# Optimization experiments

Measured on AMD Instinct MI355X. Metric: run time of the kernel, lower is better.

The kernel has to match this reference:

```python
import jax, jax.numpy as jnp
import numpy as np

NUM_HEADS = 8
HEAD_DIM = 64      # key_dim = tts_embed_dims // num_heads
TOKEN_NUM = 10
EMBED_DIMS = 512   # tts_embed_dims (num_units)
QUERY_DIM = 256    # tts_embed_dims // 2
BATCH = 131072


def setup_inputs() -> dict:
    key = jax.random.key(0)
    k1, k2, k3, k4 = jax.random.split(key, 4)
    inputs = jax.random.normal(k1, (BATCH, QUERY_DIM), dtype=jnp.float32)
    # nn.Parameter init.normal_(mean=0, std=0.5)
    embed = 0.5 * jax.random.normal(k2, (TOKEN_NUM, HEAD_DIM), dtype=jnp.float32)
    # nn.Linear weights are [out_features, in_features]
    Wq = jax.random.normal(k3, (EMBED_DIMS, QUERY_DIM), dtype=jnp.float32) * (QUERY_DIM ** -0.5)
    Wk = jax.random.normal(k4, (EMBED_DIMS, HEAD_DIM), dtype=jnp.float32) * (HEAD_DIM ** -0.5)
    return {"inputs": inputs, "embed": embed, "Wq": Wq, "Wk": Wk}


def reference(inputs, embed, Wq, Wk):
    # Faithful to this fork: values = raw tanh(embed) keys (W_value unused),
    # and NO softmax on the attention scores.
    N = inputs.shape[0]
    h, d, T = NUM_HEADS, HEAD_DIM, TOKEN_NUM
    keys_raw = jnp.tanh(embed)                       # [T, d] (shared across batch)

    q = inputs @ Wq.T                                # [N, E]
    q = q.reshape(N, h, d)                           # split heads (T_q == 1 squeezed)

    k = keys_raw @ Wk.T                              # [T, E]
    k = k.reshape(T, h, d)                           # [T, h, d]

    scale = HEAD_DIM ** 0.5                          # self.key_dim ** 0.5
    # scores: [h, N, 1, T] -> store as [h, N, T]
    scores = jnp.einsum('nhd,thd->hnt', q, k) / scale

    # out per head: scores @ values, values = keys_raw [T, d]
    out = jnp.einsum('hnt,td->nhd', scores, keys_raw)  # [N, h, d]
    style_embed = out.reshape(N, 1, h * d)             # concat heads -> [N, 1, E]
    attn_score = scores[:, :, None, :]                 # [h, N, 1, T]
    return style_embed, attn_score
```

## Files before the change

### kernel.cpp

```cpp
#include <hip/hip_runtime.h>
#include <math.h>

#define N_QDIM 256
#define N_EDIM 512
#define N_HEADS 8
#define N_HDIM 64
#define N_TOK 10
#define NJ 80

typedef short bf16x8 __attribute__((ext_vector_type(8)));
typedef float f32x4 __attribute__((ext_vector_type(4)));

__global__ __launch_bounds__(256) void precompute_kernel(
    const float* __restrict__ embed, const float* __restrict__ Wq,
    const float* __restrict__ Wk, unsigned short* __restrict__ WfHi,
    unsigned short* __restrict__ WfLo, float* __restrict__ keysOut)
{
    __shared__ float skeys[N_TOK * N_HDIM];
    __shared__ float sK[N_TOK * N_EDIM];
    const int tid = threadIdx.x;

    for (int i = tid; i < N_TOK * N_HDIM; i += 256) {
        float v = tanhf(embed[i]);
        skeys[i] = v;
        if (blockIdx.x == 0) keysOut[i] = v;
    }
    __syncthreads();

    for (int i = tid; i < N_TOK * N_EDIM; i += 256) {
        int t = i >> 9;
        int e = i & 511;
        float s = 0.f;
        #pragma unroll
        for (int d = 0; d < N_HDIM; d++)
            s += skeys[t * N_HDIM + d] * Wk[e * N_HDIM + d];
        sK[i] = s;
    }
    __syncthreads();

    int flat = blockIdx.x * 256 + tid;
    int e    = flat & 7;
    int lane = (flat >> 3) & 63;
    int rest = flat >> 9;
    int n    = rest % 5;
    int kb   = rest / 5;
    int c    = n * 16 + (lane & 15);
    int h    = c / N_TOK;
    int t    = c - h * N_TOK;
    int qd   = kb * 32 + (lane >> 4) * 8 + e;

    float s = 0.f;
    #pragma unroll
    for (int d = 0; d < N_HDIM; d++)
        s += Wq[(h * N_HDIM + d) * N_QDIM + qd] * sK[t * N_EDIM + h * N_HDIM + d];
    s *= 0.125f;

    unsigned int u = __float_as_uint(s);
    float rem = s - __uint_as_float(u & 0xffff0000u);
    int idx = ((kb * 5 + n) * 64 + lane) * 8 + e;
    WfHi[idx] = (unsigned short)(u >> 16);
    WfLo[idx] = (unsigned short)(__float_as_uint(rem) >> 16);
}

static __device__ __forceinline__ void splitFrag(float4 v0, float4 v1,
                                                 bf16x8& hi, bf16x8& lo)
{
    float x[8] = {v0.x, v0.y, v0.z, v0.w, v1.x, v1.y, v1.z, v1.w};
    #pragma unroll
    for (int e = 0; e < 8; e++) {
        unsigned u = __float_as_uint(x[e]);
        hi[e] = (short)(u >> 16);
        float r = x[e] - __uint_as_float(u & 0xffff0000u);
        lo[e] = (short)(__float_as_uint(r) >> 16);
    }
}

#define WAVE_LDS_FENCE() asm volatile("s_waitcnt lgkmcnt(0)" ::: "memory")

__global__ __launch_bounds__(256, 5) void main_kernel(
    const float* __restrict__ inputs, const unsigned short* __restrict__ WfHi,
    const unsigned short* __restrict__ WfLo, const float* __restrict__ keys,
    float* __restrict__ outStyle, float* __restrict__ outAttn, int N)
{
    __shared__ float sS[4][16 * 84];

    const int tid = threadIdx.x;
    const int w   = tid >> 6;
    const int l   = tid & 63;
    const int l15 = l & 15;
    const int lg  = l >> 4;
    const int rowBase = blockIdx.x * 128 + w * 32;

    const float* pa0 = inputs + (size_t)(rowBase + l15) * N_QDIM + lg * 8;
    const float* pa1 = pa0 + 16 * N_QDIM;

    f32x4 acc[2][5];
    #pragma unroll
    for (int m = 0; m < 2; m++)
        #pragma unroll
        for (int n = 0; n < 5; n++)
            acc[m][n] = (f32x4){0.f, 0.f, 0.f, 0.f};

    #pragma unroll 2
    for (int kb = 0; kb < 8; kb++) {
        const float* p0 = pa0 + kb * 32;
        const float* p1 = pa1 + kb * 32;
        float4 x0 = *(const float4*)(p0);
        float4 x1 = *(const float4*)(p0 + 4);
        float4 y0 = *(const float4*)(p1);
        float4 y1 = *(const float4*)(p1 + 4);
        bf16x8 a0h, a0l, a1h, a1l;
        splitFrag(x0, x1, a0h, a0l);
        splitFrag(y0, y1, a1h, a1l);

        const unsigned short* bh = WfHi + kb * 2560 + l * 8;
        const unsigned short* bl = WfLo + kb * 2560 + l * 8;
        #pragma unroll
        for (int n = 0; n < 5; n++) {
            bf16x8 bhi = *(const bf16x8*)(bh + n * 512);
            bf16x8 blo = *(const bf16x8*)(bl + n * 512);
            acc[0][n] = __builtin_amdgcn_mfma_f32_16x16x32_bf16(a0h, bhi, acc[0][n], 0, 0, 0);
            acc[1][n] = __builtin_amdgcn_mfma_f32_16x16x32_bf16(a1h, bhi, acc[1][n], 0, 0, 0);
            acc[0][n] = __builtin_amdgcn_mfma_f32_16x16x32_bf16(a0l, bhi, acc[0][n], 0, 0, 0);
            acc[1][n] = __builtin_amdgcn_mfma_f32_16x16x32_bf16(a1l, bhi, acc[1][n], 0, 0, 0);
            acc[0][n] = __builtin_amdgcn_mfma_f32_16x16x32_bf16(a0h, blo, acc[0][n], 0, 0, 0);
            acc[1][n] = __builtin_amdgcn_mfma_f32_16x16x32_bf16(a1h, blo, acc[1][n], 0, 0, 0);
        }
    }

    float* s = sS[w];

    #pragma unroll
    for (int n = 0; n < 5; n++)
        #pragma unroll
        for (int r = 0; r < 4; r++)
            s[(lg * 4 + r) * 84 + n * 16 + l15] = acc[0][n][r];
    WAVE_LDS_FENCE();

    float4 kr[N_TOK];
    #pragma unroll
    for (int t = 0; t < N_TOK; t++)
        kr[t] = *(const float4*)(keys + t * N_HDIM + l15 * 4);

    #pragma unroll
    for (int m = 0; m < 2; m++) {
        const int rStart = rowBase + m * 16;

        #pragma unroll
        for (int h = 0; h < N_HEADS; h++) {
            float* dst = outAttn + ((size_t)h * N + rStart) * N_TOK;
            #pragma unroll
            for (int it = 0; it < 3; it++) {
                int i = it * 64 + l;
                if (i < 16 * N_TOK) {
                    int rr = i / N_TOK;
                    int t  = i - rr * N_TOK;
                    __builtin_nontemporal_store(s[rr * 84 + h * N_TOK + t], dst + i);
                }
            }
        }

        #pragma unroll
        for (int i = 0; i < 4; i++) {
            int rr = i * 4 + lg;
            const float* srow = s + rr * 84;
            float* orow = outStyle + (size_t)(rStart + rr) * N_EDIM + l15 * 4;
            #pragma unroll
            for (int h = 0; h < N_HEADS; h++) {
                f32x4 o = {0.f, 0.f, 0.f, 0.f};
                #pragma unroll
                for (int t2 = 0; t2 < N_TOK; t2 += 2) {
                    float2 sc = *(const float2*)(srow + h * N_TOK + t2);
                    o[0] += sc.x * kr[t2].x + sc.y * kr[t2 + 1].x;
                    o[1] += sc.x * kr[t2].y + sc.y * kr[t2 + 1].y;
                    o[2] += sc.x * kr[t2].z + sc.y * kr[t2 + 1].z;
                    o[3] += sc.x * kr[t2].w + sc.y * kr[t2 + 1].w;
                }
                __builtin_nontemporal_store(o, (f32x4*)(orow + h * N_HDIM));
            }
        }

        if (m == 0) {
            WAVE_LDS_FENCE();
            #pragma unroll
            for (int n = 0; n < 5; n++)
                #pragma unroll
                for (int r = 0; r < 4; r++)
                    s[(lg * 4 + r) * 84 + n * 16 + l15] = acc[1][n][r];
            WAVE_LDS_FENCE();
        }
    }
}

extern "C" void kernel_launch(void* const* d_in, const int* in_sizes, int n_in,
                              void* d_out, int out_size, void* d_ws, size_t ws_size,
                              hipStream_t stream) {
    const float* inputs = (const float*)d_in[0];
    const float* embed  = (const float*)d_in[1];
    const float* Wq     = (const float*)d_in[2];
    const float* Wk     = (const float*)d_in[3];

    const int N = in_sizes[0] / N_QDIM;

    float* keysWs = (float*)d_ws;
    unsigned short* WfHi = (unsigned short*)((char*)d_ws + 640 * sizeof(float));
    unsigned short* WfLo = WfHi + 8 * 5 * 64 * 8;

    float* outStyle = (float*)d_out;
    float* outAttn  = outStyle + (size_t)N * N_EDIM;

    precompute_kernel<<<80, 256, 0, stream>>>(embed, Wq, Wk, WfHi, WfLo, keysWs);
    main_kernel<<<N / 128, 256, 0, stream>>>(inputs, WfHi, WfLo, keysWs, outStyle, outAttn, N);
}
```

Measured before the change: 463.8 us.

## Shrink main kernel to one wave per block handling 16 rows

Restructures the main kernel from 4-wave blocks each covering 32 rows (two MFMA row tiles) into single-wave blocks covering 16 rows, launching eight times as many blocks. This lowers register and LDS use per wave and removes the second LDS staging pass, aiming for higher occupancy and better latency hiding on the memory-bound work. In exchange, each B fragment loaded from WfHi/WfLo is reused for one row tile instead of two, which doubles weight-fragment load traffic per row, and block scheduling overhead rises.

```diff
diff --git a/kernel.cpp b/kernel.cpp
--- a/kernel.cpp
+++ b/kernel.cpp
@@ -77,41 +77,32 @@
 
 #define WAVE_LDS_FENCE() asm volatile("s_waitcnt lgkmcnt(0)" ::: "memory")
 
-__global__ __launch_bounds__(256, 5) void main_kernel(
+__global__ __launch_bounds__(64, 5) void main_kernel(
     const float* __restrict__ inputs, const unsigned short* __restrict__ WfHi,
     const unsigned short* __restrict__ WfLo, const float* __restrict__ keys,
     float* __restrict__ outStyle, float* __restrict__ outAttn, int N)
 {
-    __shared__ float sS[4][16 * 84];
+    __shared__ float s[16 * 84];
 
-    const int tid = threadIdx.x;
-    const int w   = tid >> 6;
-    const int l   = tid & 63;
+    const int l   = threadIdx.x;
     const int l15 = l & 15;
     const int lg  = l >> 4;
-    const int rowBase = blockIdx.x * 128 + w * 32;
+    const int rowBase = blockIdx.x * 16;
 
     const float* pa0 = inputs + (size_t)(rowBase + l15) * N_QDIM + lg * 8;
-    const float* pa1 = pa0 + 16 * N_QDIM;
 
-    f32x4 acc[2][5];
+    f32x4 acc[5];
     #pragma unroll
-    for (int m = 0; m < 2; m++)
-        #pragma unroll
-        for (int n = 0; n < 5; n++)
-            acc[m][n] = (f32x4){0.f, 0.f, 0.f, 0.f};
+    for (int n = 0; n < 5; n++)
+        acc[n] = (f32x4){0.f, 0.f, 0.f, 0.f};
 
-    #pragma unroll 2
+    #pragma unroll 4
     for (int kb = 0; kb < 8; kb++) {
         const float* p0 = pa0 + kb * 32;
-        const float* p1 = pa1 + kb * 32;
         float4 x0 = *(const float4*)(p0);
         float4 x1 = *(const float4*)(p0 + 4);
-        float4 y0 = *(const float4*)(p1);
-        float4 y1 = *(const float4*)(p1 + 4);
-        bf16x8 a0h, a0l, a1h, a1l;
-        splitFrag(x0, x1, a0h, a0l);
-        splitFrag(y0, y1, a1h, a1l);
+        bf16x8 ah, al;
+        splitFrag(x0, x1, ah, al);
 
         const unsigned short* bh = WfHi + kb * 2560 + l * 8;
         const unsigned short* bl = WfLo + kb * 2560 + l * 8;
@@ -119,22 +110,17 @@
         for (int n = 0; n < 5; n++) {
             bf16x8 bhi = *(const bf16x8*)(bh + n * 512);
             bf16x8 blo = *(const bf16x8*)(bl + n * 512);
-            acc[0][n] = __builtin_amdgcn_mfma_f32_16x16x32_bf16(a0h, bhi, acc[0][n], 0, 0, 0);
-            acc[1][n] = __builtin_amdgcn_mfma_f32_16x16x32_bf16(a1h, bhi, acc[1][n], 0, 0, 0);
-            acc[0][n] = __builtin_amdgcn_mfma_f32_16x16x32_bf16(a0l, bhi, acc[0][n], 0, 0, 0);
-            acc[1][n] = __builtin_amdgcn_mfma_f32_16x16x32_bf16(a1l, bhi, acc[1][n], 0, 0, 0);
-            acc[0][n] = __builtin_amdgcn_mfma_f32_16x16x32_bf16(a0h, blo, acc[0][n], 0, 0, 0);
-            acc[1][n] = __builtin_amdgcn_mfma_f32_16x16x32_bf16(a1h, blo, acc[1][n], 0, 0, 0);
+            acc[n] = __builtin_amdgcn_mfma_f32_16x16x32_bf16(ah, bhi, acc[n], 0, 0, 0);
+            acc[n] = __builtin_amdgcn_mfma_f32_16x16x32_bf16(al, bhi, acc[n], 0, 0, 0);
+            acc[n] = __builtin_amdgcn_mfma_f32_16x16x32_bf16(ah, blo, acc[n], 0, 0, 0);
         }
     }
-
-    float* s = sS[w];
 
     #pragma unroll
     for (int n = 0; n < 5; n++)
         #pragma unroll
         for (int r = 0; r < 4; r++)
-            s[(lg * 4 + r) * 84 + n * 16 + l15] = acc[0][n][r];
+            s[(lg * 4 + r) * 84 + n * 16 + l15] = acc[n][r];
     WAVE_LDS_FENCE();
 
     float4 kr[N_TOK];
@@ -143,51 +129,36 @@
         kr[t] = *(const float4*)(keys + t * N_HDIM + l15 * 4);
 
     #pragma unroll
-    for (int m = 0; m < 2; m++) {
-        const int rStart = rowBase + m * 16;
+    for (int h = 0; h < N_HEADS; h++) {
+        float* dst = outAttn + ((size_t)h * N + rowBase) * N_TOK;
+        #pragma unroll
+        for (int it = 0; it < 3; it++) {
+            int i = it * 64 + l;
+            if (i < 16 * N_TOK) {
+                int rr = i / N_TOK;
+                int t  = i - rr * N_TOK;
+                __builtin_nontemporal_store(s[rr * 84 + h * N_TOK + t], dst + i);
+            }
+        }
+    }
 
+    #pragma unroll
+    for (int i = 0; i < 4; i++) {
+        int rr = i * 4 + lg;
+        const float* srow = s + rr * 84;
+        float* orow = outStyle + (size_t)(rowBase + rr) * N_EDIM + l15 * 4;
         #pragma unroll
         for (int h = 0; h < N_HEADS; h++) {
-            float* dst = outAttn + ((size_t)h * N + rStart) * N_TOK;
+            f32x4 o = {0.f, 0.f, 0.f, 0.f};
             #pragma unroll
-            for (int it = 0; it < 3; it++) {
-                int i = it * 64 + l;
-                if (i < 16 * N_TOK) {
-                    int rr = i / N_TOK;
-                    int t  = i - rr * N_TOK;
-                    __builtin_nontemporal_store(s[rr * 84 + h * N_TOK + t], dst + i);
-                }
+            for (int t2 = 0; t2 < N_TOK; t2 += 2) {
+                float2 sc = *(const float2*)(srow + h * N_TOK + t2);
+                o[0] += sc.x * kr[t2].x + sc.y * kr[t2 + 1].x;
+                o[1] += sc.x * kr[t2].y + sc.y * kr[t2 + 1].y;
+                o[2] += sc.x * kr[t2].z + sc.y * kr[t2 + 1].z;
+                o[3] += sc.x * kr[t2].w + sc.y * kr[t2 + 1].w;
             }
-        }
-
-        #pragma unroll
-        for (int i = 0; i < 4; i++) {
-            int rr = i * 4 + lg;
-            const float* srow = s + rr * 84;
-            float* orow = outStyle + (size_t)(rStart + rr) * N_EDIM + l15 * 4;
-            #pragma unroll
-            for (int h = 0; h < N_HEADS; h++) {
-                f32x4 o = {0.f, 0.f, 0.f, 0.f};
-                #pragma unroll
-                for (int t2 = 0; t2 < N_TOK; t2 += 2) {
-                    float2 sc = *(const float2*)(srow + h * N_TOK + t2);
-                    o[0] += sc.x * kr[t2].x + sc.y * kr[t2 + 1].x;
-                    o[1] += sc.x * kr[t2].y + sc.y * kr[t2 + 1].y;
-                    o[2] += sc.x * kr[t2].z + sc.y * kr[t2 + 1].z;
-                    o[3] += sc.x * kr[t2].w + sc.y * kr[t2 + 1].w;
-                }
-                __builtin_nontemporal_store(o, (f32x4*)(orow + h * N_HDIM));
-            }
-        }
-
-        if (m == 0) {
-            WAVE_LDS_FENCE();
-            #pragma unroll
-            for (int n = 0; n < 5; n++)
-                #pragma unroll
-                for (int r = 0; r < 4; r++)
-                    s[(lg * 4 + r) * 84 + n * 16 + l15] = acc[1][n][r];
-            WAVE_LDS_FENCE();
+            __builtin_nontemporal_store(o, (f32x4*)(orow + h * N_HDIM));
         }
     }
 }
@@ -210,5 +181,5 @@
     float* outAttn  = outStyle + (size_t)N * N_EDIM;
 
     precompute_kernel<<<80, 256, 0, stream>>>(embed, Wq, Wk, WfHi, WfLo, keysWs);
-    main_kernel<<<N / 128, 256, 0, stream>>>(inputs, WfHi, WfLo, keysWs, outStyle, outAttn, N);
+    main_kernel<<<N / 16, 64, 0, stream>>>(inputs, WfHi, WfLo, keysWs, outStyle, outAttn, N);
 }
```

Result: no change. 467.4 us (+0.8%).
